# Optimization experiments

Hardware: AMD Instinct MI355X
Metric: run time of the kernel (lower is better)

The kernel has to match this reference:

```python
import jax, jax.numpy as jnp
import numpy as np

C = 36   # num_classes
H = 256  # hidden_dim


def setup_inputs() -> dict:
    key = jax.random.key(0)
    ks = jax.random.split(key, 12)
    B, L, Dl, Dg = 32, 196, 1024, 1024
    s = lambda d: 1.0 / np.sqrt(d)
    return {
        "local_features": jax.random.normal(ks[0], (B, L, Dl), jnp.float32),
        "global_average_pool": jax.random.normal(ks[1], (B, Dg), jnp.float32),
        "Wl": jax.random.normal(ks[2], (Dl, C * H), jnp.float32) * s(Dl),
        "bl": jax.random.normal(ks[3], (C * H,), jnp.float32) * s(Dl),
        "Wg": jax.random.normal(ks[4], (Dg, C * H), jnp.float32) * s(Dg),
        "bg": jax.random.normal(ks[5], (C * H,), jnp.float32) * s(Dg),
        "Wh": jax.random.normal(ks[6], (H, H), jnp.float32) * s(H),
        "bh": jax.random.normal(ks[7], (H,), jnp.float32) * s(H),
        "Wr": jax.random.normal(ks[8], (H, 4), jnp.float32) * s(H),
        "br": jax.random.normal(ks[9], (4,), jnp.float32) * s(H),
        "Wc": jax.random.normal(ks[10], (H, 1), jnp.float32) * s(H),
        "bc": jax.random.normal(ks[11], (1,), jnp.float32) * s(H),
    }


def reference(local_features, global_average_pool, Wl, bl, Wg, bg, Wh, bh, Wr, br, Wc, bc):
    B, L, _ = local_features.shape
    # global projection -> [B, C, H]
    xg = (global_average_pool @ Wg + bg).reshape(B, C, H)
    # local projection -> [B, L, C, H] -> [B, C, L, H]
    xl = (local_features @ Wl + bl).reshape(B, L, C, H).transpose(0, 2, 1, 3)
    # per-class attention scores over locations: [B, C, L]
    dot = jnp.einsum('bch,bclh->bcl', xg, xl)
    attn = jax.nn.softmax(dot, axis=-1)
    # attention-weighted sum over locations: [B, C, H]
    ws = jnp.einsum('bcl,bclh->bch', attn, xl)
    hid = jax.nn.relu(ws @ Wh + bh)
    bbox_coords = (hid @ Wr + br).reshape(B, C * 4)   # [B, 4C]
    bbox_presence = (hid @ Wc + bc)[..., 0]           # [B, C]
    return bbox_coords, bbox_presence
```

## Files before the change

### kernel.cpp

```cpp
#include <hip/hip_runtime.h>
#include <stdint.h>

#define NCLS 36
#define HDIM 256
#define BSZ  32
#define LLOC 196
#define DIN  1024
#define NCH  9216
#define NCH4 2304
#define XG_N 294912
#define SC_N 225792
#define SC_N4 56448
#define V_N  1179648

__device__ __forceinline__ void fma4(float4& a, float s, const float4& b) {
  a.x += s * b.x; a.y += s * b.y; a.z += s * b.z; a.w += s * b.w;
}
__device__ __forceinline__ float dot4(const float4& a, const float4& b) {
  return a.x * b.x + a.y * b.y + a.z * b.z + a.w * b.w;
}

__global__ __launch_bounds__(256) void kA_xg(
    const float* __restrict__ Wg, const float* __restrict__ gap,
    float* __restrict__ XGP) {
  __shared__ __align__(16) float4 gs[512];
  __shared__ __align__(16) float4 red[4096];
  const int tid = threadIdx.x;
  const int nt = blockIdx.x, ks = blockIdx.y;
  const int n0 = nt * 256, k0 = ks * 64;
  const float4* gap4 = (const float4*)gap;
  for (int i = tid; i < 512; i += 256)
    gs[i] = gap4[(size_t)(i >> 4) * 256 + ks * 16 + (i & 15)];
  __syncthreads();
  const int w = tid >> 6, lane = tid & 63;
  float4 acc[32] = {};
  const float* wp = Wg + (size_t)(k0 + w * 16) * NCH + n0 + lane * 4;
  for (int kq = 0; kq < 4; ++kq) {
    float4 wr[4];
    #pragma unroll
    for (int kk = 0; kk < 4; ++kk)
      wr[kk] = *(const float4*)(wp + (size_t)(kq * 4 + kk) * NCH);
    const int k4g = w * 4 + kq;
    #pragma unroll
    for (int b = 0; b < 32; ++b) {
      float4 g = gs[b * 16 + k4g];
      fma4(acc[b], g.x, wr[0]); fma4(acc[b], g.y, wr[1]);
      fma4(acc[b], g.z, wr[2]); fma4(acc[b], g.w, wr[3]);
    }
  }
  __syncthreads();
  if (w >= 2) {
    #pragma unroll
    for (int b = 0; b < 32; ++b) red[(w - 2) * 2048 + b * 64 + lane] = acc[b];
  }
  __syncthreads();
  if (w < 2) {
    #pragma unroll
    for (int b = 0; b < 32; ++b) {
      float4 t = red[w * 2048 + b * 64 + lane];
      acc[b].x += t.x; acc[b].y += t.y; acc[b].z += t.z; acc[b].w += t.w;
    }
    #pragma unroll
    for (int b = 0; b < 32; ++b) red[w * 2048 + b * 64 + lane] = acc[b];
  }
  __syncthreads();
  #pragma unroll
  for (int i = 0; i < 8; ++i) {
    int b = w * 8 + i;
    float4 a = red[b * 64 + lane];
    float4 c = red[2048 + b * 64 + lane];
    a.x += c.x; a.y += c.y; a.z += c.z; a.w += c.w;
    *(float4*)&XGP[(size_t)ks * XG_N + (size_t)b * NCH + n0 + lane * 4] = a;
  }
}

__global__ __launch_bounds__(256) void kB_red(
    const float* __restrict__ XGP, const float* __restrict__ bg,
    float* __restrict__ XG) {
  const int b = blockIdx.x / 9;
  const int j = (blockIdx.x % 9) * 256 + threadIdx.x;
  const size_t off = (size_t)b * NCH4 + j;
  const float4* p4 = (const float4*)XGP;
  float4 s = ((const float4*)bg)[j];
  #pragma unroll
  for (int p = 0; p < 16; ++p) {
    float4 t = p4[(size_t)p * (XG_N / 4) + off];
    s.x += t.x; s.y += t.y; s.z += t.z; s.w += t.w;
  }
  ((float4*)XG)[off] = s;
}

__global__ __launch_bounds__(128) void kC_V(
    const float* __restrict__ Wl, const float* __restrict__ XG,
    float* __restrict__ V) {
  __shared__ __align__(16) float4 xs[2048];
  const int tid = threadIdx.x;
  const int c = blockIdx.x, kt = blockIdx.y;
  const int k0 = kt * 32;
  const float4* xg4 = (const float4*)XG;
  for (int i = tid; i < 2048; i += 128) {
    int b = i >> 6, h4 = i & 63;
    xs[i] = xg4[(size_t)b * NCH4 + c * 64 + h4];
  }
  __syncthreads();
  const int lane = tid & 63, wv_ = tid >> 6;
  const int q = lane & 3, r = lane >> 2;
  const int b0 = wv_ * 16;
  const int krow = k0 + r * 2;
  float acc0[16] = {}; float acc1[16] = {};
  const float* wl = Wl + (size_t)krow * NCH + c * 256 + q * 4;
  #pragma unroll 4
  for (int it = 0; it < 16; ++it) {
    float4 w0 = *(const float4*)(wl + it * 16);
    float4 w1 = *(const float4*)(wl + NCH + it * 16);
    #pragma unroll
    for (int bb = 0; bb < 16; ++bb) {
      float4 x = xs[(b0 + bb) * 64 + it * 4 + q];
      acc0[bb] += dot4(w0, x);
      acc1[bb] += dot4(w1, x);
    }
  }
  #pragma unroll
  for (int bb = 0; bb < 16; ++bb) {
    float s0 = acc0[bb], s1 = acc1[bb];
    s0 += __shfl_xor(s0, 1); s0 += __shfl_xor(s0, 2);
    s1 += __shfl_xor(s1, 1); s1 += __shfl_xor(s1, 2);
    acc0[bb] = s0; acc1[bb] = s1;
  }
  if (q == 0) {
    #pragma unroll
    for (int bb = 0; bb < 16; ++bb) {
      size_t o = (size_t)((b0 + bb) * NCLS + c) * DIN + krow;
      V[o]     = acc0[bb];
      V[o + 1] = acc1[bb];
    }
  }
}

__global__ __launch_bounds__(256) void kD_scores(
    const float* __restrict__ local_f, const float* __restrict__ V,
    float* __restrict__ SCP) {
  __shared__ __align__(16) float4 loc_s[3136];
  __shared__ __align__(16) float4 v_s[576];
  const int tid = threadIdx.x;
  const int b = blockIdx.x, ks = blockIdx.y;
  const float4* lf4 = (const float4*)local_f;
  for (int i = tid; i < 3136; i += 256) {
    int r = i >> 4, g = i & 15;
    loc_s[r * 16 + ((g + r) & 15)] = lf4[(size_t)(b * LLOC + r) * 256 + ks * 16 + g];
  }
  const float4* v4 = (const float4*)V;
  for (int i = tid; i < 576; i += 256) {
    int cc = i >> 4, g = i & 15;
    v_s[i] = v4[(size_t)(b * NCLS + cc) * 256 + ks * 16 + g];
  }
  __syncthreads();
  const int lg = tid & 63, cg = tid >> 6;
  float acc[4][9] = {};
  for (int k4 = 0; k4 < 16; ++k4) {
    float4 vv[9];
    #pragma unroll
    for (int ci = 0; ci < 9; ++ci) vv[ci] = v_s[(cg * 9 + ci) * 16 + k4];
    #pragma unroll
    for (int i = 0; i < 4; ++i) {
      int l = lg + 64 * i;
      if (l < LLOC) {
        float4 a = loc_s[l * 16 + ((k4 + l) & 15)];
        #pragma unroll
        for (int ci = 0; ci < 9; ++ci) acc[i][ci] += dot4(a, vv[ci]);
      }
    }
  }
  #pragma unroll
  for (int i = 0; i < 4; ++i) {
    int l = lg + 64 * i;
    if (l < LLOC) {
      #pragma unroll
      for (int ci = 0; ci < 9; ++ci)
        SCP[(size_t)ks * SC_N + (size_t)(b * NCLS + cg * 9 + ci) * LLOC + l] = acc[i][ci];
    }
  }
}

__global__ __launch_bounds__(64) void kE_softmax(
    const float* __restrict__ SCP, float* __restrict__ ATT) {
  const int b = blockIdx.x, c = blockIdx.y, t = threadIdx.x;
  const size_t base4 = (size_t)(b * NCLS + c) * 49;
  const float4* s4 = (const float4*)SCP;
  float4 s = {0.f, 0.f, 0.f, 0.f};
  float m = -1e30f;
  if (t < 49) {
    s = s4[base4 + t];
    #pragma unroll
    for (int p = 1; p < 16; ++p) {
      float4 x = s4[(size_t)p * SC_N4 + base4 + t];
      s.x += x.x; s.y += x.y; s.z += x.z; s.w += x.w;
    }
    m = fmaxf(fmaxf(s.x, s.y), fmaxf(s.z, s.w));
  }
  #pragma unroll
  for (int off = 32; off >= 1; off >>= 1) m = fmaxf(m, __shfl_xor(m, off));
  float4 e = {0.f, 0.f, 0.f, 0.f};
  float sum = 0.f;
  if (t < 49) {
    e.x = __expf(s.x - m); e.y = __expf(s.y - m);
    e.z = __expf(s.z - m); e.w = __expf(s.w - m);
    sum = e.x + e.y + e.z + e.w;
  }
  #pragma unroll
  for (int off = 32; off >= 1; off >>= 1) sum += __shfl_xor(sum, off);
  float inv = 1.0f / sum;
  if (t < 49) {
    e.x *= inv; e.y *= inv; e.z *= inv; e.w *= inv;
    ((float4*)ATT)[base4 + t] = e;
  }
}

__global__ __launch_bounds__(256) void kF_U(
    const float* __restrict__ local_f, const float* __restrict__ ATT,
    float* __restrict__ U) {
  __shared__ __align__(16) float4 att_s[1764];
  __shared__ __align__(16) float4 red[4608];
  const int tid = threadIdx.x;
  const int b = blockIdx.x, ks = blockIdx.y;
  const int k0 = ks * 128;
  const float4* at4 = (const float4*)ATT;
  for (int i = tid; i < 1764; i += 256) {
    int cc = i / 49, l4 = i - cc * 49;
    att_s[i] = at4[(size_t)(b * NCLS + cc) * 49 + l4];
  }
  __syncthreads();
  const int kg = tid & 15, cg = (tid >> 4) & 3, lh = tid >> 6;
  float4 acc[9][2] = {};
  const float* lbase = local_f + (size_t)b * LLOC * DIN + k0 + kg * 8;
  for (int l4 = lh; l4 < 49; l4 += 4) {
    float4 lv[4][2];
    #pragma unroll
    for (int ll = 0; ll < 4; ++ll) {
      const float* p = lbase + (size_t)(l4 * 4 + ll) * DIN;
      lv[ll][0] = *(const float4*)p;
      lv[ll][1] = *(const float4*)(p + 4);
    }
    #pragma unroll
    for (int ci = 0; ci < 9; ++ci) {
      float4 av = att_s[(cg * 9 + ci) * 49 + l4];
      fma4(acc[ci][0], av.x, lv[0][0]); fma4(acc[ci][1], av.x, lv[0][1]);
      fma4(acc[ci][0], av.y, lv[1][0]); fma4(acc[ci][1], av.y, lv[1][1]);
      fma4(acc[ci][0], av.z, lv[2][0]); fma4(acc[ci][1], av.z, lv[2][1]);
      fma4(acc[ci][0], av.w, lv[3][0]); fma4(acc[ci][1], av.w, lv[3][1]);
    }
  }
  #pragma unroll
  for (int ci = 0; ci < 9; ++ci) {
    int c = cg * 9 + ci;
    red[lh * 1152 + c * 32 + kg * 2 + 0] = acc[ci][0];
    red[lh * 1152 + c * 32 + kg * 2 + 1] = acc[ci][1];
  }
  __syncthreads();
  float4* u4 = (float4*)U;
  for (int i = tid; i < 1152; i += 256) {
    float4 s = red[i];
    #pragma unroll
    for (int p = 1; p < 4; ++p) {
      float4 t = red[p * 1152 + i];
      s.x += t.x; s.y += t.y; s.z += t.z; s.w += t.w;
    }
    u4[(size_t)(b * NCLS + (i >> 5)) * 256 + ks * 32 + (i & 31)] = s;
  }
}

__global__ __launch_bounds__(256) void kG_ws(
    const float* __restrict__ Wl, const float* __restrict__ U,
    float* __restrict__ WSP) {
  __shared__ __align__(16) float4 us[512];
  __shared__ __align__(16) float4 red[4096];
  const int tid = threadIdx.x;
  const int c = blockIdx.x, ks = blockIdx.y;
  const int k0 = ks * 64;
  const float4* u4 = (const float4*)U;
  for (int i = tid; i < 512; i += 256)
    us[i] = u4[(size_t)((i >> 4) * NCLS + c) * 256 + ks * 16 + (i & 15)];
  __syncthreads();
  const int w = tid >> 6, lane = tid & 63;
  float4 acc[32] = {};
  const float* wp = Wl + (size_t)(k0 + w * 16) * NCH + c * HDIM + lane * 4;
  for (int kq = 0; kq < 4; ++kq) {
    float4 wr[4];
    #pragma unroll
    for (int kk = 0; kk < 4; ++kk)
      wr[kk] = *(const float4*)(wp + (size_t)(kq * 4 + kk) * NCH);
    const int k4g = w * 4 + kq;
    #pragma unroll
    for (int b = 0; b < 32; ++b) {
      float4 g = us[b * 16 + k4g];
      fma4(acc[b], g.x, wr[0]); fma4(acc[b], g.y, wr[1]);
      fma4(acc[b], g.z, wr[2]); fma4(acc[b], g.w, wr[3]);
    }
  }
  __syncthreads();
  if (w >= 2) {
    #pragma unroll
    for (int b = 0; b < 32; ++b) red[(w - 2) * 2048 + b * 64 + lane] = acc[b];
  }
  __syncthreads();
  if (w < 2) {
    #pragma unroll
    for (int b = 0; b < 32; ++b) {
      float4 t = red[w * 2048 + b * 64 + lane];
      acc[b].x += t.x; acc[b].y += t.y; acc[b].z += t.z; acc[b].w += t.w;
    }
    #pragma unroll
    for (int b = 0; b < 32; ++b) red[w * 2048 + b * 64 + lane] = acc[b];
  }
  __syncthreads();
  #pragma unroll
  for (int i = 0; i < 8; ++i) {
    int b = w * 8 + i;
    float4 a = red[b * 64 + lane];
    float4 cc = red[2048 + b * 64 + lane];
    a.x += cc.x; a.y += cc.y; a.z += cc.z; a.w += cc.w;
    *(float4*)&WSP[(size_t)ks * XG_N + (size_t)b * NCH + c * HDIM + lane * 4] = a;
  }
}

__global__ __launch_bounds__(256) void kH_heads(
    const float* __restrict__ Wh, const float* __restrict__ bh,
    const float* __restrict__ Wr, const float* __restrict__ br,
    const float* __restrict__ Wc, const float* __restrict__ bc,
    const float* __restrict__ bl,
    const float* __restrict__ WSP, float* __restrict__ out) {
  __shared__ float ws_s[3][HDIM];
  __shared__ float hid_s[3][HDIM];
  const int b = blockIdx.x, c0 = blockIdx.y * 3;
  const int j = threadIdx.x;
  #pragma unroll
  for (int ci = 0; ci < 3; ++ci) {
    size_t base = (size_t)b * NCH + (c0 + ci) * HDIM + j;
    float s = bl[(c0 + ci) * HDIM + j];
    #pragma unroll
    for (int p = 0; p < 16; ++p) s += WSP[(size_t)p * XG_N + base];
    ws_s[ci][j] = s;
  }
  __syncthreads();
  float acc[3] = {0, 0, 0};
  for (int h = 0; h < HDIM; ++h) {
    float whj = Wh[(size_t)h * HDIM + j];
    acc[0] += ws_s[0][h] * whj;
    acc[1] += ws_s[1][h] * whj;
    acc[2] += ws_s[2][h] * whj;
  }
  float bj = bh[j];
  #pragma unroll
  for (int ci = 0; ci < 3; ++ci) hid_s[ci][j] = fmaxf(acc[ci] + bj, 0.0f);
  __syncthreads();
  const int r = j >> 6, j0 = j & 63;
  for (int ci = 0; ci < 3; ++ci) {
    const int c = c0 + ci;
    float s = 0.f;
    #pragma unroll
    for (int m = 0; m < 4; ++m)
      s += hid_s[ci][j0 + 64 * m] * Wr[(j0 + 64 * m) * 4 + r];
    #pragma unroll
    for (int off = 32; off >= 1; off >>= 1) s += __shfl_xor(s, off);
    if (j0 == 0) out[(size_t)b * (NCLS * 4) + c * 4 + r] = s + br[r];
    if (r == 0) {
      float p = 0.f;
      #pragma unroll
      for (int m = 0; m < 4; ++m)
        p += hid_s[ci][j0 + 64 * m] * Wc[j0 + 64 * m];
      #pragma unroll
      for (int off = 32; off >= 1; off >>= 1) p += __shfl_xor(p, off);
      if (j0 == 0) out[BSZ * NCLS * 4 + b * NCLS + c] = p + bc[0];
    }
  }
}

extern "C" void kernel_launch(void* const* d_in, const int* in_sizes, int n_in,
                              void* d_out, int out_size, void* d_ws, size_t ws_size,
                              hipStream_t stream) {
  const float* local = (const float*)d_in[0];
  const float* gap   = (const float*)d_in[1];
  const float* Wl    = (const float*)d_in[2];
  const float* bl    = (const float*)d_in[3];
  const float* Wg    = (const float*)d_in[4];
  const float* bg    = (const float*)d_in[5];
  const float* Wh    = (const float*)d_in[6];
  const float* bh    = (const float*)d_in[7];
  const float* Wr    = (const float*)d_in[8];
  const float* br    = (const float*)d_in[9];
  const float* Wc    = (const float*)d_in[10];
  const float* bc    = (const float*)d_in[11];
  float* out         = (float*)d_out;

  float* XGP = (float*)d_ws;
  float* XG  = XGP + (size_t)16 * XG_N;
  float* V   = XG + XG_N;
  float* SCP = V + V_N;
  float* ATT = SCP + (size_t)16 * SC_N;
  float* U   = ATT + SC_N;
  float* WSP = U + V_N;

  kA_xg     <<<dim3(36, 16), dim3(256), 0, stream>>>(Wg, gap, XGP);
  kB_red    <<<dim3(288),    dim3(256), 0, stream>>>(XGP, bg, XG);
  kC_V      <<<dim3(36, 32), dim3(128), 0, stream>>>(Wl, XG, V);
  kD_scores <<<dim3(32, 16), dim3(256), 0, stream>>>(local, V, SCP);
  kE_softmax<<<dim3(32, 36), dim3(64),  0, stream>>>(SCP, ATT);
  kF_U      <<<dim3(32, 8),  dim3(256), 0, stream>>>(local, ATT, U);
  kG_ws     <<<dim3(36, 16), dim3(256), 0, stream>>>(Wl, U, WSP);
  kH_heads  <<<dim3(32, 12), dim3(256), 0, stream>>>(Wh, bh, Wr, br, Wc, bc, bl, WSP, out);
}
```

Baseline: 267.9 us.

## Restructure kC_V to stage Wl tiles in LDS with split-H reduction

The kernel computing V = XG·Wl^T per class now loads a 64-row Wl tile into swizzled shared memory instead of streaming it from global memory per thread. Each of four waves handles a quarter of the hidden dimension and computes a 4x8 (k, batch) register tile, and partial sums are combined through shared memory before coalesced float4 stores. The grid halves and block size doubles. This aims to improve Wl reuse and coalesced writes, at the cost of 96KB of LDS per block (lower occupancy) and extra sync/reduction steps.

Result: slower. 280.5 us (+4.7%).

```diff
diff --git a/kernel.cpp b/kernel.cpp
--- a/kernel.cpp
+++ b/kernel.cpp
@@ -90,50 +90,72 @@
   ((float4*)XG)[off] = s;
 }
 
-__global__ __launch_bounds__(128) void kC_V(
+__global__ __launch_bounds__(256) void kC_V(
     const float* __restrict__ Wl, const float* __restrict__ XG,
     float* __restrict__ V) {
-  __shared__ __align__(16) float4 xs[2048];
+  __shared__ __align__(16) float4 wl_s[4096];
+  __shared__ __align__(16) float4 xg_s[2048];
   const int tid = threadIdx.x;
   const int c = blockIdx.x, kt = blockIdx.y;
-  const int k0 = kt * 32;
+  const int k0 = kt * 64;
+  for (int i = tid; i < 4096; i += 256) {
+    int r = i >> 6, g = i & 63;
+    wl_s[r * 64 + ((g + r) & 63)] =
+        *(const float4*)&Wl[(size_t)(k0 + r) * NCH + c * 256 + g * 4];
+  }
   const float4* xg4 = (const float4*)XG;
-  for (int i = tid; i < 2048; i += 128) {
+  for (int i = tid; i < 2048; i += 256) {
     int b = i >> 6, h4 = i & 63;
-    xs[i] = xg4[(size_t)b * NCH4 + c * 64 + h4];
-  }
-  __syncthreads();
-  const int lane = tid & 63, wv_ = tid >> 6;
-  const int q = lane & 3, r = lane >> 2;
-  const int b0 = wv_ * 16;
-  const int krow = k0 + r * 2;
-  float acc0[16] = {}; float acc1[16] = {};
-  const float* wl = Wl + (size_t)krow * NCH + c * 256 + q * 4;
-  #pragma unroll 4
-  for (int it = 0; it < 16; ++it) {
-    float4 w0 = *(const float4*)(wl + it * 16);
-    float4 w1 = *(const float4*)(wl + NCH + it * 16);
-    #pragma unroll
-    for (int bb = 0; bb < 16; ++bb) {
-      float4 x = xs[(b0 + bb) * 64 + it * 4 + q];
-      acc0[bb] += dot4(w0, x);
-      acc1[bb] += dot4(w1, x);
-    }
-  }
-  #pragma unroll
-  for (int bb = 0; bb < 16; ++bb) {
-    float s0 = acc0[bb], s1 = acc1[bb];
-    s0 += __shfl_xor(s0, 1); s0 += __shfl_xor(s0, 2);
-    s1 += __shfl_xor(s1, 1); s1 += __shfl_xor(s1, 2);
-    acc0[bb] = s0; acc1[bb] = s1;
-  }
-  if (q == 0) {
-    #pragma unroll
-    for (int bb = 0; bb < 16; ++bb) {
-      size_t o = (size_t)((b0 + bb) * NCLS + c) * DIN + krow;
-      V[o]     = acc0[bb];
-      V[o + 1] = acc1[bb];
-    }
+    xg_s[b * 64 + ((h4 + (b >> 3)) & 63)] = xg4[(size_t)b * NCH4 + c * 64 + h4];
+  }
+  __syncthreads();
+  const int w = tid >> 6, lane = tid & 63;
+  const int k16 = lane & 15;
+  const int bslot = lane >> 4;
+  const int b0 = bslot * 8;
+  float acc[4][8] = {};
+  for (int h4 = w * 16; h4 < w * 16 + 16; ++h4) {
+    float4 wv[4];
+    #pragma unroll
+    for (int kk = 0; kk < 4; ++kk) {
+      int k = k16 + 16 * kk;
+      wv[kk] = wl_s[k * 64 + ((h4 + k) & 63)];
+    }
+    const int xcol = (h4 + bslot) & 63;
+    #pragma unroll
+    for (int bb = 0; bb < 8; ++bb) {
+      float4 x = xg_s[(b0 + bb) * 64 + xcol];
+      #pragma unroll
+      for (int kk = 0; kk < 4; ++kk) acc[kk][bb] += dot4(wv[kk], x);
+    }
+  }
+  __syncthreads();
+  float* red = (float*)wl_s;
+  if (w >= 2) {
+    #pragma unroll
+    for (int kk = 0; kk < 4; ++kk)
+      #pragma unroll
+      for (int bb = 0; bb < 8; ++bb)
+        red[(w - 2) * 2048 + (b0 + bb) * 64 + k16 + 16 * kk] = acc[kk][bb];
+  }
+  __syncthreads();
+  if (w < 2) {
+    #pragma unroll
+    for (int kk = 0; kk < 4; ++kk)
+      #pragma unroll
+      for (int bb = 0; bb < 8; ++bb) {
+        int o = w * 2048 + (b0 + bb) * 64 + k16 + 16 * kk;
+        red[o] += acc[kk][bb];
+      }
+  }
+  __syncthreads();
+  const float4* r04 = (const float4*)red;
+  float4* v4 = (float4*)V;
+  for (int i = tid; i < 512; i += 256) {
+    float4 a = r04[i], bv = r04[512 + i];
+    a.x += bv.x; a.y += bv.y; a.z += bv.z; a.w += bv.w;
+    int b = i >> 4, kq = i & 15;
+    v4[(size_t)(b * NCLS + c) * 256 + kt * 16 + kq] = a;
   }
 }
 
@@ -402,7 +424,7 @@
 
   kA_xg     <<<dim3(36, 16), dim3(256), 0, stream>>>(Wg, gap, XGP);
   kB_red    <<<dim3(288),    dim3(256), 0, stream>>>(XGP, bg, XG);
-  kC_V      <<<dim3(36, 32), dim3(128), 0, stream>>>(Wl, XG, V);
+  kC_V      <<<dim3(36, 16), dim3(256), 0, stream>>>(Wl, XG, V);
   kD_scores <<<dim3(32, 16), dim3(256), 0, stream>>>(local, V, SCP);
   kE_softmax<<<dim3(32, 36), dim3(64),  0, stream>>>(SCP, ATT);
   kF_U      <<<dim3(32, 8),  dim3(256), 0, stream>>>(local, ATT, U);
```

## Restructure kC_V tiling with 8-row register blocking and transpose-reduce shuffles

Applied to the files above, without the earlier changes.

Rewrites the kernel that computes V = Wl·xg per class so that each thread holds 8 Wl rows by 16 batches in registers, with 16 lanes spanning h instead of 4. A butterfly transpose-reduce across shuffle stages leaves each lane with a full sum for one batch, which removes the redundant shuffle work and the q==0-only stores. The block size doubles to 256 with 64 k-rows per block and half the grid. The aim is better reuse of each xs element from shared memory and less shuffle overhead, at the cost of higher register pressure (128 accumulators) and strided scalar stores to V.

New measurement: 258.3 us. 3.6% less time.

```diff
diff --git a/kernel.cpp b/kernel.cpp
--- a/kernel.cpp
+++ b/kernel.cpp
@@ -90,51 +90,86 @@
   ((float4*)XG)[off] = s;
 }
 
-__global__ __launch_bounds__(128) void kC_V(
+__global__ __launch_bounds__(256, 2) void kC_V(
     const float* __restrict__ Wl, const float* __restrict__ XG,
     float* __restrict__ V) {
   __shared__ __align__(16) float4 xs[2048];
   const int tid = threadIdx.x;
   const int c = blockIdx.x, kt = blockIdx.y;
-  const int k0 = kt * 32;
   const float4* xg4 = (const float4*)XG;
-  for (int i = tid; i < 2048; i += 128) {
+  for (int i = tid; i < 2048; i += 256) {
     int b = i >> 6, h4 = i & 63;
     xs[i] = xg4[(size_t)b * NCH4 + c * 64 + h4];
   }
   __syncthreads();
-  const int lane = tid & 63, wv_ = tid >> 6;
-  const int q = lane & 3, r = lane >> 2;
-  const int b0 = wv_ * 16;
-  const int krow = k0 + r * 2;
-  float acc0[16] = {}; float acc1[16] = {};
-  const float* wl = Wl + (size_t)krow * NCH + c * 256 + q * 4;
-  #pragma unroll 4
-  for (int it = 0; it < 16; ++it) {
-    float4 w0 = *(const float4*)(wl + it * 16);
-    float4 w1 = *(const float4*)(wl + NCH + it * 16);
-    #pragma unroll
-    for (int bb = 0; bb < 16; ++bb) {
-      float4 x = xs[(b0 + bb) * 64 + it * 4 + q];
-      acc0[bb] += dot4(w0, x);
-      acc1[bb] += dot4(w1, x);
-    }
-  }
-  #pragma unroll
-  for (int bb = 0; bb < 16; ++bb) {
-    float s0 = acc0[bb], s1 = acc1[bb];
-    s0 += __shfl_xor(s0, 1); s0 += __shfl_xor(s0, 2);
-    s1 += __shfl_xor(s1, 1); s1 += __shfl_xor(s1, 2);
-    acc0[bb] = s0; acc1[bb] = s1;
-  }
-  if (q == 0) {
-    #pragma unroll
-    for (int bb = 0; bb < 16; ++bb) {
-      size_t o = (size_t)((b0 + bb) * NCLS + c) * DIN + krow;
-      V[o]     = acc0[bb];
-      V[o + 1] = acc1[bb];
-    }
-  }
+  const int w = tid >> 6, lane = tid & 63;
+  const int h16 = lane & 15, r4 = lane >> 4;
+  const int kh = w & 1, bh = w >> 1;
+  const int kbase = kt * 64 + kh * 32 + r4;
+  float acc[8][16] = {};
+  const float* wp = Wl + (size_t)kbase * NCH + c * 256 + h16 * 4;
+  for (int it = 0; it < 4; ++it) {
+    float4 wv[8];
+    #pragma unroll
+    for (int kk = 0; kk < 8; ++kk)
+      wv[kk] = *(const float4*)(wp + (size_t)(kk * 4) * NCH + it * 64);
+    #pragma unroll
+    for (int b = 0; b < 16; ++b) {
+      float4 x = xs[(bh * 16 + b) * 64 + it * 16 + h16];
+      #pragma unroll
+      for (int kk = 0; kk < 8; ++kk) acc[kk][b] += dot4(wv[kk], x);
+    }
+  }
+  float f1[8][8];
+  {
+    const bool hb = h16 & 1;
+    #pragma unroll
+    for (int kk = 0; kk < 8; ++kk)
+      #pragma unroll
+      for (int j = 0; j < 8; ++j) {
+        float keep = hb ? acc[kk][2 * j + 1] : acc[kk][2 * j];
+        float send = hb ? acc[kk][2 * j]     : acc[kk][2 * j + 1];
+        f1[kk][j] = keep + __shfl_xor(send, 1);
+      }
+  }
+  float f2[8][4];
+  {
+    const bool hb = (h16 >> 1) & 1;
+    #pragma unroll
+    for (int kk = 0; kk < 8; ++kk)
+      #pragma unroll
+      for (int j = 0; j < 4; ++j) {
+        float keep = hb ? f1[kk][2 * j + 1] : f1[kk][2 * j];
+        float send = hb ? f1[kk][2 * j]     : f1[kk][2 * j + 1];
+        f2[kk][j] = keep + __shfl_xor(send, 2);
+      }
+  }
+  float f3[8][2];
+  {
+    const bool hb = (h16 >> 2) & 1;
+    #pragma unroll
+    for (int kk = 0; kk < 8; ++kk)
+      #pragma unroll
+      for (int j = 0; j < 2; ++j) {
+        float keep = hb ? f2[kk][2 * j + 1] : f2[kk][2 * j];
+        float send = hb ? f2[kk][2 * j]     : f2[kk][2 * j + 1];
+        f3[kk][j] = keep + __shfl_xor(send, 4);
+      }
+  }
+  float f4v[8];
+  {
+    const bool hb = (h16 >> 3) & 1;
+    #pragma unroll
+    for (int kk = 0; kk < 8; ++kk) {
+      float keep = hb ? f3[kk][1] : f3[kk][0];
+      float send = hb ? f3[kk][0] : f3[kk][1];
+      f4v[kk] = keep + __shfl_xor(send, 8);
+    }
+  }
+  const int b = bh * 16 + h16;
+  float* vp = V + (size_t)(b * NCLS + c) * DIN + kbase;
+  #pragma unroll
+  for (int kk = 0; kk < 8; ++kk) vp[kk * 4] = f4v[kk];
 }
 
 __global__ __launch_bounds__(256) void kD_scores(
@@ -402,7 +437,7 @@
 
   kA_xg     <<<dim3(36, 16), dim3(256), 0, stream>>>(Wg, gap, XGP);
   kB_red    <<<dim3(288),    dim3(256), 0, stream>>>(XGP, bg, XG);
-  kC_V      <<<dim3(36, 32), dim3(128), 0, stream>>>(Wl, XG, V);
+  kC_V      <<<dim3(36, 16), dim3(256), 0, stream>>>(Wl, XG, V);
   kD_scores <<<dim3(32, 16), dim3(256), 0, stream>>>(local, V, SCP);
   kE_softmax<<<dim3(32, 36), dim3(64),  0, stream>>>(SCP, ATT);
   kF_U      <<<dim3(32, 8),  dim3(256), 0, stream>>>(local, ATT, U);
```
